# Optimization experiments

Measured on AMD Instinct MI355X. Metric: run time of the kernel, lower is better.

## Reference

```python
import jax, jax.numpy as jnp
import numpy as np

N_VIEWS = 2
TEMPERATURE = 0.07


def setup_inputs() -> dict:
    key = jax.random.key(0)
    # concatenated features for n_views=2 views of batch_size=4096, proj dim 128
    features = jax.random.normal(key, (8192, 128), dtype=jnp.float32)
    return {"features": features}


def reference(features) -> jnp.ndarray:
    # NT-Xent / SimCLR loss, faithful to the torch module:
    #   sim = F F^T ; drop diagonal ; logits = [positive, negatives] / T ;
    #   CE with label 0  ==  mean( logsumexp(off_diag/T) - positive/T )
    # (concatenating [pos, neg] is a row permutation of the off-diagonal
    #  entries, and CrossEntropy(label=0) only needs logsumexp(row) - pos.)
    N = features.shape[0]
    B = N // N_VIEWS
    inv_t = 1.0 / TEMPERATURE

    sim = jnp.matmul(features, features.T)  # [N, N]

    row = jnp.arange(N)
    # off-diagonal column indices in increasing-j order, matching mask.view:
    # cols[i] = [0..i-1, i+1..N-1]
    cols = jnp.arange(N - 1)[None, :]
    cols = cols + (cols >= row[:, None])  # [N, N-1]
    sim_offdiag = jnp.take_along_axis(sim, cols, axis=1)  # [N, N-1]

    # with n_views=2 the single positive for row i is its other view (i+B) % N
    pos = sim[row, (row + B) % N]  # [N]

    lse = jax.nn.logsumexp(sim_offdiag * inv_t, axis=1)  # [N]
    loss = jnp.mean(lse - pos * inv_t)
    return loss
```

## Files before the change

kernel.cpp:

```cpp
#include <hip/hip_runtime.h>
#include <math.h>

typedef __bf16 bf16x8 __attribute__((ext_vector_type(8)));
typedef float f32x4 __attribute__((ext_vector_type(4)));
typedef unsigned short u16x8 __attribute__((ext_vector_type(8)));

#define N_TOT 8192
#define HALF_N 4096
#define D 128
#define INV_T 14.285714285714286f
#define CSC 20.609929155556627f
#define NCSC -20.609929155556627f
#define LN2F 0.69314718055994531f
#define NEG_BIG -3.0e38f
#define M_INIT -1.0e30f
#define THR_RAW 1.0f
#define CS 16

__device__ __forceinline__ unsigned short f2bf(float f) {
    union { float f; unsigned int u; } a; a.f = f;
    unsigned int u = a.u;
    return (unsigned short)((u + 0x7fffu + ((u >> 16) & 1u)) >> 16);
}

__global__ __launch_bounds__(256)
void cvt_kernel(const float* __restrict__ in, unsigned short* __restrict__ fbP) {
    const int c   = blockIdx.x * 256 + threadIdx.x;
    const int q   = c >> 6;
    const int rem = c & 63;
    const int lg  = rem >> 4, lr = rem & 15;
    const int kk  = q & 3;
    const int col = (q >> 2) * 16 + lr;
    const int j16 = kk * 4 + lg;
    const float4 v0 = reinterpret_cast<const float4*>(in)[col * 32 + j16 * 2];
    const float4 v1 = reinterpret_cast<const float4*>(in)[col * 32 + j16 * 2 + 1];
    u16x8 o;
    o[0] = f2bf(v0.x); o[1] = f2bf(v0.y); o[2] = f2bf(v0.z); o[3] = f2bf(v0.w);
    o[4] = f2bf(v1.x); o[5] = f2bf(v1.y); o[6] = f2bf(v1.z); o[7] = f2bf(v1.w);
    reinterpret_cast<u16x8*>(fbP)[c] = o;
}

__global__ __launch_bounds__(256, 3)
void simclr_kernel(const unsigned short* __restrict__ fbP,
                   float* __restrict__ pm, float* __restrict__ ps,
                   float* __restrict__ rowpos) {
    __shared__ __align__(16) unsigned short lds[2][4096];
    const int tid  = threadIdx.x;
    const int lane = tid & 63;
    const int wid  = tid >> 6;
    const int lr   = lane & 15;
    const int lg   = lane >> 4;
    const int RT0  = blockIdx.x * 16 + wid * 4;
    const int Tw   = blockIdx.y * 32;

    bf16x8 br[4][4];
#pragma unroll
    for (int rt = 0; rt < 4; ++rt)
#pragma unroll
        for (int kk = 0; kk < 4; ++kk)
            br[rt][kk] = *reinterpret_cast<const bf16x8*>(
                fbP + ((size_t)(((RT0 + rt) * 4 + kk) * 64) + lane) * 8);

    float m[4], s[4];
#pragma unroll
    for (int rt = 0; rt < 4; ++rt) { m[rt] = M_INIT; s[rt] = 0.f; }

    auto stage = [&](int p, int b) {
#pragma unroll
        for (int h = 0; h < 2; ++h) {
            const unsigned short* src =
                fbP + ((size_t)(Tw + 2 * p) * 256 + h * 256 + tid) * 8;
            unsigned short* dst = &lds[b][(h * 256 + tid) * 8];
            __builtin_amdgcn_global_load_lds(
                (const __attribute__((address_space(1))) unsigned int*)(const void*)src,
                (__attribute__((address_space(3))) unsigned int*)(void*)dst,
                16, 0, 0);
        }
    };

    stage(0, 0);
    __syncthreads();

    int buf = 0;
#pragma unroll 1
    for (int p = 0; p < 16; ++p) {
        if (p < 15) stage(p + 1, buf ^ 1);

        bf16x8 ca[4], cb[4];
#pragma unroll
        for (int kk = 0; kk < 4; ++kk) {
            ca[kk] = *reinterpret_cast<const bf16x8*>(&lds[buf][(kk * 64 + lane) * 8]);
            cb[kk] = *reinterpret_cast<const bf16x8*>(&lds[buf][((kk + 4) * 64 + lane) * 8]);
        }

        const int c0 = blockIdx.y * 512 + p * 32;

        f32x4 accP[4], accQ[4];
#pragma unroll
        for (int rt = 0; rt < 4; ++rt) accP[rt] = f32x4{0.f, 0.f, 0.f, 0.f};
#pragma unroll
        for (int kk = 0; kk < 4; ++kk)
#pragma unroll
            for (int rt = 0; rt < 4; ++rt)
                accP[rt] = __builtin_amdgcn_mfma_f32_16x16x32_bf16(ca[kk], br[rt][kk], accP[rt], 0, 0, 0);
#pragma unroll
        for (int rt = 0; rt < 4; ++rt) accQ[rt] = f32x4{0.f, 0.f, 0.f, 0.f};
#pragma unroll
        for (int kk = 0; kk < 4; ++kk)
#pragma unroll
            for (int rt = 0; rt < 4; ++rt)
                accQ[rt] = __builtin_amdgcn_mfma_f32_16x16x32_bf16(cb[kk], br[rt][kk], accQ[rt], 0, 0, 0);

#pragma unroll
        for (int rt = 0; rt < 4; ++rt) {
            const int rowbase = (RT0 + rt) * 16;
            f32x4 P = accP[rt], Q = accQ[rt];
            if (c0 == (rowbase ^ HALF_N)) {
#pragma unroll
                for (int r = 0; r < 4; ++r)
                    if (lr == lg * 4 + r) rowpos[rowbase + lr] = P[r];
            }
            if (c0 + 16 == (rowbase ^ HALF_N)) {
#pragma unroll
                for (int r = 0; r < 4; ++r)
                    if (lr == lg * 4 + r) rowpos[rowbase + lr] = Q[r];
            }
            if (c0 == rowbase) {
#pragma unroll
                for (int r = 0; r < 4; ++r)
                    if (lr == lg * 4 + r) P[r] = NEG_BIG;
            }
            if (c0 + 16 == rowbase) {
#pragma unroll
                for (int r = 0; r < 4; ++r)
                    if (lr == lg * 4 + r) Q[r] = NEG_BIG;
            }
            const float t1 = fmaxf(fmaxf(P[0], P[1]), P[2]);
            const float t2 = fmaxf(fmaxf(P[3], Q[0]), Q[1]);
            const float t3 = fmaxf(Q[2], Q[3]);
            const float rmax = fmaxf(fmaxf(t1, t2), t3);
            if (!__all(rmax <= m[rt] + THR_RAW)) {
                const float mn = fmaxf(m[rt], rmax);
                s[rt] *= __builtin_amdgcn_exp2f(fmaf(m[rt], CSC, mn * NCSC));
                m[rt] = mn;
            }
            const float cm = m[rt] * NCSC;
            const float e0 = __builtin_amdgcn_exp2f(fmaf(P[0], CSC, cm));
            const float e1 = __builtin_amdgcn_exp2f(fmaf(P[1], CSC, cm));
            const float e2 = __builtin_amdgcn_exp2f(fmaf(P[2], CSC, cm));
            const float e3 = __builtin_amdgcn_exp2f(fmaf(P[3], CSC, cm));
            const float e4 = __builtin_amdgcn_exp2f(fmaf(Q[0], CSC, cm));
            const float e5 = __builtin_amdgcn_exp2f(fmaf(Q[1], CSC, cm));
            const float e6 = __builtin_amdgcn_exp2f(fmaf(Q[2], CSC, cm));
            const float e7 = __builtin_amdgcn_exp2f(fmaf(Q[3], CSC, cm));
            s[rt] += ((e0 + e1) + (e2 + e3)) + ((e4 + e5) + (e6 + e7));
        }

        __syncthreads();
        buf ^= 1;
    }

#pragma unroll
    for (int rt = 0; rt < 4; ++rt) {
        float M = m[rt];
        M = fmaxf(M, __shfl_xor(M, 16, 64));
        M = fmaxf(M, __shfl_xor(M, 32, 64));
        float sc = s[rt] * __builtin_amdgcn_exp2f(fmaf(m[rt], CSC, M * NCSC));
        sc += __shfl_xor(sc, 16, 64);
        sc += __shfl_xor(sc, 32, 64);
        if (lg == 0) {
            const int row = (RT0 + rt) * 16 + lr;
            pm[blockIdx.y * N_TOT + row] = M;
            ps[blockIdx.y * N_TOT + row] = sc;
        }
    }
}

__global__ __launch_bounds__(256)
void rowloss_mean_kernel(const float* __restrict__ pm, const float* __restrict__ ps,
                         const float* __restrict__ rowpos, float* __restrict__ out) {
    const int row = blockIdx.x * 256 + threadIdx.x;
    float M = pm[row], S = ps[row];
#pragma unroll
    for (int c = 1; c < CS; ++c) {
        const float Mo = pm[c * N_TOT + row], So = ps[c * N_TOT + row];
        const float mn = fmaxf(M, Mo);
        S = fmaf(S,  __builtin_amdgcn_exp2f(fmaf(M,  CSC, mn * NCSC)),
                 So * __builtin_amdgcn_exp2f(fmaf(Mo, CSC, mn * NCSC)));
        M = mn;
    }
    float acc = LN2F * fmaf(M, CSC, __builtin_amdgcn_logf(S)) - rowpos[row] * INV_T;
#pragma unroll
    for (int off = 32; off > 0; off >>= 1) acc += __shfl_xor(acc, off, 64);
    __shared__ float ls[4];
    if ((threadIdx.x & 63) == 0) ls[threadIdx.x >> 6] = acc;
    __syncthreads();
    if (threadIdx.x == 0)
        atomicAdd(out, (ls[0] + ls[1] + ls[2] + ls[3]) * (1.0f / (float)N_TOT));
}

extern "C" void kernel_launch(void* const* d_in, const int* in_sizes, int n_in,
                              void* d_out, int out_size, void* d_ws, size_t ws_size,
                              hipStream_t stream) {
    const float* feat = (const float*)d_in[0];
    char* ws = (char*)d_ws;
    unsigned short* fbP = (unsigned short*)ws;
    float* pm      = (float*)(ws + (size_t)N_TOT * D * 2);
    float* ps      = (float*)(ws + (size_t)N_TOT * D * 2 + (size_t)CS * N_TOT * 4);
    float* rowpos  = (float*)(ws + (size_t)N_TOT * D * 2 + 2 * (size_t)CS * N_TOT * 4);
    float* out = (float*)d_out;

    hipMemsetAsync(out, 0, sizeof(float), stream);
    cvt_kernel<<<512, 256, 0, stream>>>(feat, fbP);
    simclr_kernel<<<dim3(32, CS), 256, 0, stream>>>(fbP, pm, ps, rowpos);
    rowloss_mean_kernel<<<N_TOT / 256, 256, 0, stream>>>(pm, ps, rowpos, out);
}
```

Measured before the change: 42.78 us.

## Skip exp work on tiles well below running max and halve column tiles

Each iteration now handles 16 columns instead of 32. The column range is split across 32 grid slices instead of 16, and occupancy is raised to 4 blocks per CU with half the LDS. A wave-uniform test skips the exp2 and accumulation for a tile when every value sits more than 1.5 raw units below the running row max. The aim is to remove most of the transcendental work in the softmax epilogue and to improve latency hiding. The cost is that skipped terms are dropped, which gives a tiny approximation error, and the reduce kernel must merge twice as many partial (max, sum) pairs.

```diff
diff --git a/kernel.cpp b/kernel.cpp
--- a/kernel.cpp
+++ b/kernel.cpp
@@ -15,7 +15,8 @@
 #define NEG_BIG -3.0e38f
 #define M_INIT -1.0e30f
 #define THR_RAW 1.0f
-#define CS 16
+#define SKIP_RAW 1.5f
+#define CS 32
 
 __device__ __forceinline__ unsigned short f2bf(float f) {
     union { float f; unsigned int u; } a; a.f = f;
@@ -40,18 +41,18 @@
     reinterpret_cast<u16x8*>(fbP)[c] = o;
 }
 
-__global__ __launch_bounds__(256, 3)
+__global__ __launch_bounds__(256, 4)
 void simclr_kernel(const unsigned short* __restrict__ fbP,
                    float* __restrict__ pm, float* __restrict__ ps,
                    float* __restrict__ rowpos) {
-    __shared__ __align__(16) unsigned short lds[2][4096];
+    __shared__ __align__(16) unsigned short lds[2][2048];
     const int tid  = threadIdx.x;
     const int lane = tid & 63;
     const int wid  = tid >> 6;
     const int lr   = lane & 15;
     const int lg   = lane >> 4;
     const int RT0  = blockIdx.x * 16 + wid * 4;
-    const int Tw   = blockIdx.y * 32;
+    const int Tw   = blockIdx.y * 16;
 
     bf16x8 br[4][4];
 #pragma unroll
@@ -65,17 +66,13 @@
 #pragma unroll
     for (int rt = 0; rt < 4; ++rt) { m[rt] = M_INIT; s[rt] = 0.f; }
 
-    auto stage = [&](int p, int b) {
-#pragma unroll
-        for (int h = 0; h < 2; ++h) {
-            const unsigned short* src =
-                fbP + ((size_t)(Tw + 2 * p) * 256 + h * 256 + tid) * 8;
-            unsigned short* dst = &lds[b][(h * 256 + tid) * 8];
-            __builtin_amdgcn_global_load_lds(
-                (const __attribute__((address_space(1))) unsigned int*)(const void*)src,
-                (__attribute__((address_space(3))) unsigned int*)(void*)dst,
-                16, 0, 0);
-        }
+    auto stage = [&](int t, int b) {
+        const unsigned short* src = fbP + ((size_t)(Tw + t) * 256 + tid) * 8;
+        unsigned short* dst = &lds[b][tid * 8];
+        __builtin_amdgcn_global_load_lds(
+            (const __attribute__((address_space(1))) unsigned int*)(const void*)src,
+            (__attribute__((address_space(3))) unsigned int*)(void*)dst,
+            16, 0, 0);
     };
 
     stage(0, 0);
@@ -83,77 +80,53 @@
 
     int buf = 0;
 #pragma unroll 1
-    for (int p = 0; p < 16; ++p) {
-        if (p < 15) stage(p + 1, buf ^ 1);
+    for (int t = 0; t < 16; ++t) {
+        if (t < 15) stage(t + 1, buf ^ 1);
 
-        bf16x8 ca[4], cb[4];
+        bf16x8 ca[4];
 #pragma unroll
-        for (int kk = 0; kk < 4; ++kk) {
+        for (int kk = 0; kk < 4; ++kk)
             ca[kk] = *reinterpret_cast<const bf16x8*>(&lds[buf][(kk * 64 + lane) * 8]);
-            cb[kk] = *reinterpret_cast<const bf16x8*>(&lds[buf][((kk + 4) * 64 + lane) * 8]);
-        }
 
-        const int c0 = blockIdx.y * 512 + p * 32;
+        const int c0 = blockIdx.y * 256 + t * 16;
 
-        f32x4 accP[4], accQ[4];
+        f32x4 acc[4];
 #pragma unroll
-        for (int rt = 0; rt < 4; ++rt) accP[rt] = f32x4{0.f, 0.f, 0.f, 0.f};
+        for (int rt = 0; rt < 4; ++rt) acc[rt] = f32x4{0.f, 0.f, 0.f, 0.f};
 #pragma unroll
         for (int kk = 0; kk < 4; ++kk)
 #pragma unroll
             for (int rt = 0; rt < 4; ++rt)
-                accP[rt] = __builtin_amdgcn_mfma_f32_16x16x32_bf16(ca[kk], br[rt][kk], accP[rt], 0, 0, 0);
-#pragma unroll
-        for (int rt = 0; rt < 4; ++rt) accQ[rt] = f32x4{0.f, 0.f, 0.f, 0.f};
-#pragma unroll
-        for (int kk = 0; kk < 4; ++kk)
-#pragma unroll
-            for (int rt = 0; rt < 4; ++rt)
-                accQ[rt] = __builtin_amdgcn_mfma_f32_16x16x32_bf16(cb[kk], br[rt][kk], accQ[rt], 0, 0, 0);
+                acc[rt] = __builtin_amdgcn_mfma_f32_16x16x32_bf16(ca[kk], br[rt][kk], acc[rt], 0, 0, 0);
 
 #pragma unroll
         for (int rt = 0; rt < 4; ++rt) {
             const int rowbase = (RT0 + rt) * 16;
-            f32x4 P = accP[rt], Q = accQ[rt];
+            f32x4 P = acc[rt];
             if (c0 == (rowbase ^ HALF_N)) {
 #pragma unroll
                 for (int r = 0; r < 4; ++r)
                     if (lr == lg * 4 + r) rowpos[rowbase + lr] = P[r];
-            }
-            if (c0 + 16 == (rowbase ^ HALF_N)) {
-#pragma unroll
-                for (int r = 0; r < 4; ++r)
-                    if (lr == lg * 4 + r) rowpos[rowbase + lr] = Q[r];
             }
             if (c0 == rowbase) {
 #pragma unroll
                 for (int r = 0; r < 4; ++r)
                     if (lr == lg * 4 + r) P[r] = NEG_BIG;
             }
-            if (c0 + 16 == rowbase) {
-#pragma unroll
-                for (int r = 0; r < 4; ++r)
-                    if (lr == lg * 4 + r) Q[r] = NEG_BIG;
+            const float rmax = fmaxf(fmaxf(P[0], P[1]), fmaxf(P[2], P[3]));
+            if (!__all(rmax <= m[rt] - SKIP_RAW)) {
+                if (!__all(rmax <= m[rt] + THR_RAW)) {
+                    const float mn = fmaxf(m[rt], rmax);
+                    s[rt] *= __builtin_amdgcn_exp2f(fmaf(m[rt], CSC, mn * NCSC));
+                    m[rt] = mn;
+                }
+                const float cm = m[rt] * NCSC;
+                const float e0 = __builtin_amdgcn_exp2f(fmaf(P[0], CSC, cm));
+                const float e1 = __builtin_amdgcn_exp2f(fmaf(P[1], CSC, cm));
+                const float e2 = __builtin_amdgcn_exp2f(fmaf(P[2], CSC, cm));
+                const float e3 = __builtin_amdgcn_exp2f(fmaf(P[3], CSC, cm));
+                s[rt] += (e0 + e1) + (e2 + e3);
             }
-            const float t1 = fmaxf(fmaxf(P[0], P[1]), P[2]);
-            const float t2 = fmaxf(fmaxf(P[3], Q[0]), Q[1]);
-            const float t3 = fmaxf(Q[2], Q[3]);
-            const float rmax = fmaxf(fmaxf(t1, t2), t3);
-            if (!__all(rmax <= m[rt] + THR_RAW)) {
-                const float mn = fmaxf(m[rt], rmax);
-                s[rt] *= __builtin_amdgcn_exp2f(fmaf(m[rt], CSC, mn * NCSC));
-                m[rt] = mn;
-            }
-            const float cm = m[rt] * NCSC;
-            const float e0 = __builtin_amdgcn_exp2f(fmaf(P[0], CSC, cm));
-            const float e1 = __builtin_amdgcn_exp2f(fmaf(P[1], CSC, cm));
-            const float e2 = __builtin_amdgcn_exp2f(fmaf(P[2], CSC, cm));
-            const float e3 = __builtin_amdgcn_exp2f(fmaf(P[3], CSC, cm));
-            const float e4 = __builtin_amdgcn_exp2f(fmaf(Q[0], CSC, cm));
-            const float e5 = __builtin_amdgcn_exp2f(fmaf(Q[1], CSC, cm));
-            const float e6 = __builtin_amdgcn_exp2f(fmaf(Q[2], CSC, cm));
-            const float e7 = __builtin_amdgcn_exp2f(fmaf(Q[3], CSC, cm));
-            s[rt] += ((e0 + e1) + (e2 + e3)) + ((e4 + e5) + (e6 + e7));
         }
 
         __syncthreads();
```

After: 49.89 us. 1.17x slower.
